# Performance work log

Hardware: AMD Instinct MI355X
Metric: run time of the kernel (lower is better)

The kernel has to match this reference:

```python
import jax, jax.numpy as jnp
import numpy as np

NC, NPR, E, B = 200000, 100000, 500000, 200000
DIN, HID, HEADS = 16, 256, 8
D = HID // HEADS
NCOLOR, NSIZE, NGROUP = 1000, 30, 50


def setup_inputs() -> dict:
    key = jax.random.key(0)
    ks = jax.random.split(key, 24)
    g = lambda i, shape, s=0.05: jax.random.normal(ks[i], shape, jnp.float32) * s
    return dict(
        customer_x=g(0, (NC, DIN), 1.0),
        product_x=g(1, (NPR, DIN), 1.0),
        proj_cust_W=g(2, (DIN, HID)), proj_cust_b=jnp.zeros((HID,), jnp.float32),
        proj_prod_W=g(3, (DIN, HID)), proj_prod_b=jnp.zeros((HID,), jnp.float32),
        att_src_r=g(4, (HEADS, D)), att_dst_r=g(5, (HEADS, D)),
        att_src_rb=g(6, (HEADS, D)), att_dst_rb=g(7, (HEADS, D)),
        q_sem=g(8, (HID,)), k_lin_W=g(9, (HID, HID)), k_lin_b=jnp.zeros((HID,), jnp.float32),
        color_emb=g(10, (NCOLOR, 8), 1.0),
        size_emb=g(11, (NSIZE, 4), 1.0),
        group_emb=g(12, (NGROUP, 4), 1.0),
        fc1_W=g(13, (HID * 2 + 16, 128)), fc1_b=jnp.zeros((128,), jnp.float32),
        fc2_W=g(14, (128, 32)), fc2_b=jnp.zeros((32,), jnp.float32),
        fc3_W=g(15, (32, 1)), fc3_b=jnp.zeros((1,), jnp.float32),
        bn1_gamma=jnp.ones((128,), jnp.float32), bn1_beta=jnp.zeros((128,), jnp.float32),
        bn2_gamma=jnp.ones((32,), jnp.float32), bn2_beta=jnp.zeros((32,), jnp.float32),
        edge_src=jax.random.randint(ks[16], (E,), 0, NC),
        edge_dst=jax.random.randint(ks[17], (E,), 0, NPR),
        label_src=jax.random.randint(ks[18], (B,), 0, NC),
        label_dst=jax.random.randint(ks[19], (B,), 0, NPR),
        size_idx=jax.random.randint(ks[20], (B,), 0, NSIZE),
        color_idx=jax.random.randint(ks[21], (B,), 0, NCOLOR),
        group_idx=jax.random.randint(ks[22], (B,), 0, NGROUP),
    )


def _edge_softmax(logits, dst, n):
    # destination-grouped softmax over edges; logits: [E,H]
    m = jax.ops.segment_max(logits, dst, num_segments=n)
    m = jnp.where(jnp.isfinite(m), m, 0.0)
    e = jnp.exp(logits - m[dst])
    s = jax.ops.segment_sum(e, dst, num_segments=n)
    return e / (s[dst] + 1e-16)


def _han_relation(h_src, h_dst, a_src, a_dst, src, dst, n_dst):
    # h_*: [N,H,D]; a_*: [H,D]
    logits = (h_src * a_src).sum(-1)[src] + (h_dst * a_dst).sum(-1)[dst]  # [E,H]
    logits = jax.nn.leaky_relu(logits, 0.2)
    alpha = _edge_softmax(logits, dst, n_dst)
    msg = alpha[:, :, None] * h_src[src]  # [E,H,D]
    out = jax.ops.segment_sum(msg, dst, num_segments=n_dst)
    return jax.nn.relu(out.reshape(n_dst, -1))  # [N_dst, H*D]


def _group(outs, q, kW, kb):
    # semantic attention over metapaths (PyG HANConv group)
    stk = jnp.stack(outs)  # [M,N,F]
    score = (q * jnp.tanh(stk @ kW + kb).mean(1)).sum(-1)  # [M]
    attn = jax.nn.softmax(score)
    return jnp.einsum('m,mnf->nf', attn, stk)


def _bn(x, gamma, beta):
    mu = x.mean(0)
    var = x.var(0)
    return (x - mu) * jax.lax.rsqrt(var + 1e-5) * gamma + beta


def reference(customer_x, product_x, proj_cust_W, proj_cust_b, proj_prod_W, proj_prod_b,
              att_src_r, att_dst_r, att_src_rb, att_dst_rb, q_sem, k_lin_W, k_lin_b,
              color_emb, size_emb, group_emb, fc1_W, fc1_b, fc2_W, fc2_b, fc3_W, fc3_b,
              bn1_gamma, bn1_beta, bn2_gamma, bn2_beta,
              edge_src, edge_dst, label_src, label_dst, size_idx, color_idx, group_idx):
    h_c = (customer_x @ proj_cust_W + proj_cust_b).reshape(-1, HEADS, D)
    h_p = (product_x @ proj_prod_W + proj_prod_b).reshape(-1, HEADS, D)
    # relation customer -returns-> product
    out_p = _han_relation(h_c, h_p, att_src_r, att_dst_r, edge_src, edge_dst, NPR)
    # relation product -returned_by-> customer (reversed edges)
    out_c = _han_relation(h_p, h_c, att_src_rb, att_dst_rb, edge_dst, edge_src, NC)
    cust = _group([out_c], q_sem, k_lin_W, k_lin_b)  # [NC, 256]
    prod = _group([out_p], q_sem, k_lin_W, k_lin_b)  # [NPR, 256]
    feat = jnp.concatenate([cust[label_src], prod[label_dst],
                            size_emb[size_idx], color_emb[color_idx], group_emb[group_idx]], axis=-1)
    x = jax.nn.relu(feat @ fc1_W + fc1_b)
    x = _bn(x, bn1_gamma, bn1_beta)
    x = jax.nn.relu(x @ fc2_W + fc2_b)
    x = _bn(x, bn2_gamma, bn2_beta)
    return x @ fc3_W + fc3_b
```

## Files before the change

kernel.cpp:

```cpp
#include <hip/hip_runtime.h>

#define NCC 200000
#define NPRR 100000
#define NEE 500000
#define NBB 200000

typedef __attribute__((ext_vector_type(8))) short bf16x8;
typedef __attribute__((ext_vector_type(16))) float f32x16;

__device__ __forceinline__ float b2f(unsigned short u){ return __uint_as_float(((unsigned)u)<<16); }
__device__ __forceinline__ unsigned short f2b(float f){
  unsigned x = __float_as_uint(f);
  return (unsigned short)((x + 0x7fffu + ((x>>16)&1u)) >> 16);
}

__global__ __launch_bounds__(256) void wa_prep2(
    const float* __restrict__ Wc, const float* __restrict__ bc,
    const float* __restrict__ attAc, const float* __restrict__ attBc,
    const float* __restrict__ Wp, const float* __restrict__ bp,
    const float* __restrict__ attAp, const float* __restrict__ attBp,
    float* __restrict__ WAc, float* __restrict__ WAp)
{
  int tid = threadIdx.x;
  for (int task = tid; task < 4*17*8; task += 256) {
    int grp = task / 136, rem = task % 136;
    int k = rem >> 3, h = rem & 7;
    const float* att = (grp==0)?attAc:(grp==1)?attBc:(grp==2)?attAp:attBp;
    const float* W   = (grp<2)?Wc:Wp;
    const float* bias= (grp<2)?bc:bp;
    const float* row = (k < 16) ? (W + k*256) : bias;
    float acc = 0.f;
    for (int d = 0; d < 32; d++) acc = fmaf(row[h*32+d], att[h*32+d], acc);
    if (grp<2) WAc[(grp&1)*136 + rem] = acc;
    else       WAp[(grp&1)*136 + rem] = acc;
  }
}

__global__ __launch_bounds__(256) void prep_proj(
    const float* __restrict__ Wc, const float* __restrict__ Wp,
    const float* __restrict__ WAc, const float* __restrict__ WAp,
    unsigned short* __restrict__ WtC, unsigned short* __restrict__ WtP,
    unsigned short* __restrict__ WAtC, unsigned short* __restrict__ WAtP)
{
  int idx = blockIdx.x*256 + threadIdx.x;
  if (idx < 4096){ int n=idx>>4, k=idx&15; WtC[idx]=f2b(Wc[k*256+n]); }
  else if (idx < 8192){ int t=idx-4096; int n=t>>4, k=t&15; WtP[t]=f2b(Wp[k*256+n]); }
  else if (idx < 8704){ int t=idx-8192; int n=t>>4, k=t&15;
    WAtC[t] = (n<16)? f2b(WAc[(n>>3)*136 + k*8 + (n&7)]) : (unsigned short)0; }
  else if (idx < 9216){ int t=idx-8704; int n=t>>4, k=t&15;
    WAtP[t] = (n<16)? f2b(WAp[(n>>3)*136 + k*8 + (n&7)]) : (unsigned short)0; }
}

__global__ __launch_bounds__(256) void prep_fc1(const float* __restrict__ fc1W,
    const float* __restrict__ fc1b,
    const float* __restrict__ size_emb, const float* __restrict__ color_emb,
    const float* __restrict__ group_emb,
    unsigned short* __restrict__ BtC, unsigned short* __restrict__ BtP,
    float* __restrict__ Ts, float* __restrict__ Tc, float* __restrict__ Tg)
{
  int idx = blockIdx.x*256 + threadIdx.x;
  if (idx < 32768){
    int n = idx>>8, k = idx&255;
    BtC[idx] = f2b(fc1W[k*128 + n]);
  } else if (idx < 65536){
    int t = idx - 32768;
    int n = t>>8, k = t&255;
    BtP[t] = f2b(fc1W[(256+k)*128 + n]);
  } else if (idx < 65536 + 30*128){
    int t = idx - 65536;
    int s = t>>7, j = t&127;
    float a = fc1b[j];
    #pragma unroll
    for (int c=0;c<4;c++) a = fmaf(size_emb[s*4+c], fc1W[(512+c)*128+j], a);
    Ts[t] = a;
  } else if (idx < 65536 + 30*128 + 1000*128){
    int t = idx - 65536 - 30*128;
    int col = t>>7, j = t&127;
    float a = 0.f;
    #pragma unroll
    for (int c=0;c<8;c++) a = fmaf(color_emb[col*8+c], fc1W[(516+c)*128+j], a);
    Tc[t] = a;
  } else if (idx < 65536 + 30*128 + 1000*128 + 50*128){
    int t = idx - 65536 - 30*128 - 1000*128;
    int g = t>>7, j = t&127;
    float a = 0.f;
    #pragma unroll
    for (int c=0;c<4;c++) a = fmaf(group_emb[g*4+c], fc1W[(524+c)*128+j], a);
    Tg[t] = a;
  }
}

__global__ __launch_bounds__(256) void proj_mfma(const float* __restrict__ X,
    const unsigned short* __restrict__ Wt, const unsigned short* __restrict__ WAt,
    const float* __restrict__ WA,
    unsigned short* __restrict__ H, float* __restrict__ sA, float* __restrict__ sB,
    int N, int nt)
{
  __shared__ unsigned short wt[4608];
  __shared__ float biasS[16];
  int tid = threadIdx.x;
  for (int i=tid; i<512; i+=256) ((uint4*)wt)[i] = ((const uint4*)Wt)[i];
  for (int i=tid; i<64;  i+=256) ((uint4*)(wt+4096))[i] = ((const uint4*)WAt)[i];
  if (tid < 16) biasS[tid] = WA[(tid>>3)*136 + 128 + (tid&7)];
  __syncthreads();
  int wv = tid>>6, lane = tid&63, m = lane&31, hi = lane>>5;
  for (int t = blockIdx.x; t < nt; t += gridDim.x){
    int node = t*32 + m;
    bf16x8 a;
    {
      const float4* xr = (const float4*)(X + (long long)node*16 + hi*8);
      float4 f0 = xr[0], f1 = xr[1];
      unsigned short av[8] = {f2b(f0.x),f2b(f0.y),f2b(f0.z),f2b(f0.w),
                              f2b(f1.x),f2b(f1.y),f2b(f1.z),f2b(f1.w)};
      a = *(bf16x8*)av;
    }
    #pragma unroll
    for (int s=0;s<2;s++){
      int c0 = wv*64 + s*32;
      bf16x8 b = *(const bf16x8*)(wt + (c0+m)*16 + hi*8);
      f32x16 acc;
      #pragma unroll
      for (int i=0;i<16;i++) acc[i]=0.f;
      acc = __builtin_amdgcn_mfma_f32_32x32x16_bf16(a, b, acc, 0, 0, 0);
      #pragma unroll
      for (int reg=0; reg<16; reg++){
        int row = (reg&3) + 8*(reg>>2) + 4*hi;
        H[(long long)(t*32+row)*256 + c0 + m] = f2b(acc[reg]);
      }
    }
    if (wv == 0){
      bf16x8 b = *(const bf16x8*)(wt + 4096 + m*16 + hi*8);
      f32x16 acc;
      #pragma unroll
      for (int i=0;i<16;i++) acc[i]=0.f;
      acc = __builtin_amdgcn_mfma_f32_32x32x16_bf16(a, b, acc, 0, 0, 0);
      if (m < 16){
        float bias = biasS[m];
        float* dst = (m < 8) ? sA : sB;
        int h = m & 7;
        #pragma unroll
        for (int reg=0; reg<16; reg++){
          int row = (reg&3) + 8*(reg>>2) + 4*hi;
          dst[(long long)(t*32+row)*8 + h] = acc[reg] + bias;
        }
      }
    }
  }
}

__global__ __launch_bounds__(256) void hist2(const int* __restrict__ src, const int* __restrict__ dst,
    int* __restrict__ cnt_c, int* __restrict__ cnt_p, int E)
{
  int e = blockIdx.x*256 + threadIdx.x;
  if (e >= E) return;
  atomicAdd(&cnt_p[dst[e]], 1);
  atomicAdd(&cnt_c[src[e]], 1);
}

__global__ __launch_bounds__(256) void scan_phase1(const int* __restrict__ cnt, int* __restrict__ bsum, int N)
{
  __shared__ int red[256];
  int tid = threadIdx.x;
  int base = blockIdx.x*1024 + tid*4;
  int s = 0;
  #pragma unroll
  for (int k=0;k<4;k++){ int i=base+k; if (i<N) s += cnt[i]; }
  red[tid] = s;
  __syncthreads();
  for (int off=128; off>0; off>>=1){ if (tid<off) red[tid]+=red[tid+off]; __syncthreads(); }
  if (tid==0) bsum[blockIdx.x] = red[0];
}

__global__ __launch_bounds__(256) void scan_phase2(int* __restrict__ bsum, int B,
    int* __restrict__ rowptr, int N)
{
  __shared__ int ts[256];
  int tid = threadIdx.x;
  int v = (tid<B) ? bsum[tid] : 0;
  ts[tid] = v;
  __syncthreads();
  for (int off=1; off<256; off<<=1){
    int t = (tid>=off) ? ts[tid-off] : 0;
    __syncthreads();
    ts[tid] += t;
    __syncthreads();
  }
  if (tid < B) bsum[tid] = ts[tid] - v;
  if (tid == B-1) rowptr[N] = ts[tid];
}

__global__ __launch_bounds__(256) void scan_phase3(const int* __restrict__ cnt,
    const int* __restrict__ bsum, int* __restrict__ rowptr, int N)
{
  __shared__ int ts[256];
  int tid = threadIdx.x;
  int base = blockIdx.x*1024 + tid*4;
  int v[4]; int s = 0;
  #pragma unroll
  for (int k=0;k<4;k++){ int i=base+k; v[k] = (i<N) ? cnt[i] : 0; s += v[k]; }
  ts[tid] = s;
  __syncthreads();
  for (int off=1; off<256; off<<=1){
    int t = (tid>=off) ? ts[tid-off] : 0;
    __syncthreads();
    ts[tid] += t;
    __syncthreads();
  }
  int run = bsum[blockIdx.x] + ts[tid] - s;
  #pragma unroll
  for (int k=0;k<4;k++){ int i=base+k; if (i<N){ rowptr[i]=run; run += v[k]; } }
}

__global__ __launch_bounds__(256) void place2(const int* __restrict__ src, const int* __restrict__ dst,
    const int* __restrict__ rp_r, const int* __restrict__ rp_rb,
    int* __restrict__ cnt_p, int* __restrict__ cnt_c,
    int* __restrict__ si_r, int* __restrict__ si_rb, int E)
{
  int e = blockIdx.x*256 + threadIdx.x;
  if (e >= E) return;
  int s = src[e], d = dst[e];
  si_r [rp_r [d] + atomicAdd(&cnt_p[d], 1)] = s;
  si_rb[rp_rb[s] + atomicAdd(&cnt_c[s], 1)] = d;
}

__global__ __launch_bounds__(256) void agg_gemm(
    const int* __restrict__ rowptr, const int* __restrict__ srcidx,
    const float* __restrict__ sSrc, const float* __restrict__ sDst,
    const unsigned short* __restrict__ H, const unsigned short* __restrict__ Bt,
    unsigned short* __restrict__ Y)
{
  __shared__ unsigned short feat[32*264];
  int tid = threadIdx.x;
  int wv = tid>>6, lane = tid&63;
  int g = lane>>4, ln = lane&15, h = ln>>1;
  long long base = (long long)blockIdx.x*32;
  #pragma unroll
  for (int t=0;t<2;t++){
    int r = wv*8 + t*4 + g;
    long long n = base + r;
    int e0 = rowptr[n], e1 = rowptr[n+1];
    int elast = e1 - 1;
    float sdh = sDst[n*8 + h];
    float acc[16];
    #pragma unroll
    for (int c=0;c<16;c++) acc[c]=0.f;
    float den = 0.f;
    for (int e = e0; e < e1; e += 4){
      int i1 = min(e+1, elast), i2 = min(e+2, elast), i3 = min(e+3, elast);
      int s0 = srcidx[e],  s1 = srcidx[i1];
      int s2 = srcidx[i2], s3 = srcidx[i3];
      const uint4* p0 = (const uint4*)&H[(long long)s0*256 + ln*16];
      const uint4* p1 = (const uint4*)&H[(long long)s1*256 + ln*16];
      const uint4* p2 = (const uint4*)&H[(long long)s2*256 + ln*16];
      const uint4* p3 = (const uint4*)&H[(long long)s3*256 + ln*16];
      uint4 uA0 = p0[0], uA1 = p0[1];
      uint4 uB0 = p1[0], uB1 = p1[1];
      uint4 uC0 = p2[0], uC1 = p2[1];
      uint4 uD0 = p3[0], uD1 = p3[1];
      float l0 = sSrc[(long long)s0*8 + h];
      float l1 = sSrc[(long long)s1*8 + h];
      float l2 = sSrc[(long long)s2*8 + h];
      float l3 = sSrc[(long long)s3*8 + h];
      l0 += sdh; l1 += sdh; l2 += sdh; l3 += sdh;
      float w0 = __expf(l0 > 0.f ? l0 : 0.2f*l0);
      float w1 = (e+1 < e1) ? __expf(l1 > 0.f ? l1 : 0.2f*l1) : 0.f;
      float w2 = (e+2 < e1) ? __expf(l2 > 0.f ? l2 : 0.2f*l2) : 0.f;
      float w3 = (e+3 < e1) ? __expf(l3 > 0.f ? l3 : 0.2f*l3) : 0.f;
      den += (w0 + w1) + (w2 + w3);
      unsigned ua[8] = {uA0.x,uA0.y,uA0.z,uA0.w, uA1.x,uA1.y,uA1.z,uA1.w};
      unsigned ub[8] = {uB0.x,uB0.y,uB0.z,uB0.w, uB1.x,uB1.y,uB1.z,uB1.w};
      unsigned uc[8] = {uC0.x,uC0.y,uC0.z,uC0.w, uC1.x,uC1.y,uC1.z,uC1.w};
      unsigned ud[8] = {uD0.x,uD0.y,uD0.z,uD0.w, uD1.x,uD1.y,uD1.z,uD1.w};
      #pragma unroll
      for (int p=0;p<8;p++){
        acc[p*2]   = fmaf(w0, b2f((unsigned short)(ua[p]&0xffffu)), acc[p*2]);
        acc[p*2+1] = fmaf(w0, b2f((unsigned short)(ua[p]>>16)),     acc[p*2+1]);
        acc[p*2]   = fmaf(w1, b2f((unsigned short)(ub[p]&0xffffu)), acc[p*2]);
        acc[p*2+1] = fmaf(w1, b2f((unsigned short)(ub[p]>>16)),     acc[p*2+1]);
        acc[p*2]   = fmaf(w2, b2f((unsigned short)(uc[p]&0xffffu)), acc[p*2]);
        acc[p*2+1] = fmaf(w2, b2f((unsigned short)(uc[p]>>16)),     acc[p*2+1]);
        acc[p*2]   = fmaf(w3, b2f((unsigned short)(ud[p]&0xffffu)), acc[p*2]);
        acc[p*2+1] = fmaf(w3, b2f((unsigned short)(ud[p]>>16)),     acc[p*2+1]);
      }
    }
    float inv = 1.f/(den + 1e-16f);
    unsigned short ov[16];
    #pragma unroll
    for (int c=0;c<16;c++) ov[c] = f2b(fmaxf(acc[c]*inv, 0.f));
    *(uint4*)&feat[r*264 + ln*16]     = *(uint4*)&ov[0];
    *(uint4*)&feat[r*264 + ln*16 + 8] = *(uint4*)&ov[8];
  }
  __syncthreads();
  int m = lane&31, hi = lane>>5;
  f32x16 acc;
  #pragma unroll
  for (int i=0;i<16;i++) acc[i]=0.f;
  const unsigned short* ap  = feat + m*264 + hi*8;
  const unsigned short* btp = Bt + (wv*32 + m)*256 + hi*8;
  #pragma unroll 4
  for (int ks=0; ks<16; ks++){
    bf16x8 a = *(const bf16x8*)(ap + ks*16);
    bf16x8 b = *(const bf16x8*)(btp + ks*16);
    acc = __builtin_amdgcn_mfma_f32_32x32x16_bf16(a, b, acc, 0, 0, 0);
  }
  int col = wv*32 + m;
  #pragma unroll
  for (int reg=0; reg<16; reg++){
    int row = (reg&3) + 8*(reg>>2) + 4*hi;
    Y[(base+row)*128 + col] = f2b(acc[reg]);
  }
}

__global__ __launch_bounds__(256) void gather_fc1(
    const unsigned short* __restrict__ Yc, const unsigned short* __restrict__ Yp,
    const float* __restrict__ Ts, const float* __restrict__ Tc, const float* __restrict__ Tg,
    const int* __restrict__ lsrc, const int* __restrict__ ldst,
    const int* __restrict__ sidx, const int* __restrict__ cidx, const int* __restrict__ gidx,
    unsigned short* __restrict__ x1, float* __restrict__ bnsum, int ntiles)
{
  __shared__ float redS[16][128];
  __shared__ float redQ[16][128];
  int tid = threadIdx.x;
  int rl = tid>>4, g = tid&15;
  float sacc[8] = {0,0,0,0,0,0,0,0};
  float qacc[8] = {0,0,0,0,0,0,0,0};
  for (int t = blockIdx.x; t < ntiles; t += gridDim.x){
    long long row = (long long)t*16 + rl;
    int ls = lsrc[row], ld = ldst[row], si = sidx[row], ci = cidx[row], gi = gidx[row];
    uint4 uc = *(const uint4*)&Yc[(long long)ls*128 + g*8];
    uint4 up = *(const uint4*)&Yp[(long long)ld*128 + g*8];
    float4 t0 = *(const float4*)&Ts[si*128 + g*8];
    float4 t1 = *(const float4*)&Ts[si*128 + g*8 + 4];
    float4 c0 = *(const float4*)&Tc[ci*128 + g*8];
    float4 c1 = *(const float4*)&Tc[ci*128 + g*8 + 4];
    float4 g0 = *(const float4*)&Tg[gi*128 + g*8];
    float4 g1 = *(const float4*)&Tg[gi*128 + g*8 + 4];
    unsigned ucs[4] = {uc.x,uc.y,uc.z,uc.w};
    unsigned ups[4] = {up.x,up.y,up.z,up.w};
    float tb[8] = {t0.x+c0.x+g0.x, t0.y+c0.y+g0.y, t0.z+c0.z+g0.z, t0.w+c0.w+g0.w,
                   t1.x+c1.x+g1.x, t1.y+c1.y+g1.y, t1.z+c1.z+g1.z, t1.w+c1.w+g1.w};
    unsigned short ov[8];
    #pragma unroll
    for (int p=0;p<4;p++){
      float vl = b2f((unsigned short)(ucs[p]&0xffffu)) + b2f((unsigned short)(ups[p]&0xffffu)) + tb[p*2];
      float vh = b2f((unsigned short)(ucs[p]>>16))     + b2f((unsigned short)(ups[p]>>16))     + tb[p*2+1];
      vl = fmaxf(vl, 0.f); vh = fmaxf(vh, 0.f);
      ov[p*2] = f2b(vl); ov[p*2+1] = f2b(vh);
      sacc[p*2]   += vl; qacc[p*2]   += vl*vl;
      sacc[p*2+1] += vh; qacc[p*2+1] += vh*vh;
    }
    *(uint4*)&x1[row*128 + g*8] = *(uint4*)ov;
  }
  #pragma unroll
  for (int j=0;j<8;j++){ redS[rl][g*8+j]=sacc[j]; redQ[rl][g*8+j]=qacc[j]; }
  __syncthreads();
  if (tid < 128){
    float s=0.f, q=0.f;
    #pragma unroll
    for (int r=0;r<16;r++){ s += redS[r][tid]; q += redQ[r][tid]; }
    atomicAdd(&bnsum[tid], s);
    atomicAdd(&bnsum[128+tid], q);
  }
}

__global__ void bn1_fold(const float* __restrict__ bnsum,
    const float* __restrict__ gamma, const float* __restrict__ beta,
    const float* __restrict__ fc2W, const float* __restrict__ fc2b,
    unsigned short* __restrict__ Bt2, float* __restrict__ b2p, float invB)
{
  __shared__ float sc[128], sh[128];
  int tid = threadIdx.x;
  if (tid<128){
    float mu  = bnsum[tid]*invB;
    float var = bnsum[128+tid]*invB - mu*mu;
    float s = gamma[tid] * rsqrtf(var + 1e-5f);
    sc[tid]=s; sh[tid]= beta[tid] - mu*s;
  }
  __syncthreads();
  for (int idx=tid; idx<32*128; idx+=256){
    int n = idx>>7, k = idx&127;
    Bt2[idx] = f2b(sc[k]*fc2W[k*32+n]);
  }
  if (tid<32){
    float a = fc2b[tid];
    for (int k=0;k<128;k++) a = fmaf(sh[k], fc2W[k*32+tid], a);
    b2p[tid]=a;
  }
}

__global__ __launch_bounds__(256) void fc2_mfma(const unsigned short* __restrict__ x1,
    const unsigned short* __restrict__ Bt2, const float* __restrict__ b2p,
    unsigned short* __restrict__ x2, float* __restrict__ bnsum2, int M)
{
  __shared__ unsigned short xt[128*136];
  __shared__ unsigned short wt[32*136];
  __shared__ float redS[4][32];
  __shared__ float redQ[4][32];
  int tid = threadIdx.x;
  long long base = (long long)blockIdx.x*128;
  for (int idx=tid; idx<128*16; idx+=256){
    int r = idx>>4, c = idx&15;
    uint4 u = make_uint4(0,0,0,0);
    if (base + r < M) u = *(const uint4*)&x1[(base+r)*128 + c*8];
    *(uint4*)&xt[r*136 + c*8] = u;
  }
  for (int idx=tid; idx<32*16; idx+=256){
    int r = idx>>4, c = idx&15;
    *(uint4*)&wt[r*136 + c*8] = *(const uint4*)&Bt2[r*128 + c*8];
  }
  __syncthreads();
  int wv = tid>>6, lane = tid&63;
  int m = lane&31, hi = lane>>5;
  f32x16 acc;
  #pragma unroll
  for (int i=0;i<16;i++) acc[i]=0.f;
  const unsigned short* ap = xt + (wv*32 + m)*136 + hi*8;
  const unsigned short* bp = wt + m*136 + hi*8;
  #pragma unroll
  for (int ks=0; ks<8; ks++){
    bf16x8 a = *(const bf16x8*)(ap + ks*16);
    bf16x8 b = *(const bf16x8*)(bp + ks*16);
    acc = __builtin_amdgcn_mfma_f32_32x32x16_bf16(a, b, acc, 0, 0, 0);
  }
  int col = m;
  float bias = b2p[col];
  float s=0.f, q=0.f;
  #pragma unroll
  for (int reg=0; reg<16; reg++){
    int row = (reg&3) + 8*(reg>>2) + 4*hi;
    long long grow = base + wv*32 + row;
    float v = fmaxf(acc[reg] + bias, 0.f);
    if (grow < M) x2[grow*32 + col] = f2b(v);
    s += v; q += v*v;
  }
  if (base + 128 > M){
    s = 0.f; q = 0.f;
    #pragma unroll
    for (int reg=0; reg<16; reg++){
      int row = (reg&3) + 8*(reg>>2) + 4*hi;
      long long grow = base + wv*32 + row;
      float v = fmaxf(acc[reg] + bias, 0.f);
      if (grow < M){ s += v; q += v*v; }
    }
  }
  s += __shfl_xor(s, 32);
  q += __shfl_xor(q, 32);
  if (hi == 0){ redS[wv][col] = s; redQ[wv][col] = q; }
  __syncthreads();
  if (tid < 32){
    float a = redS[0][tid]+redS[1][tid]+redS[2][tid]+redS[3][tid];
    float b = redQ[0][tid]+redQ[1][tid]+redQ[2][tid]+redQ[3][tid];
    atomicAdd(&bnsum2[tid], a);
    atomicAdd(&bnsum2[32+tid], b);
  }
}

__global__ void bn2_fold(const float* __restrict__ bnsum2,
    const float* __restrict__ gamma2, const float* __restrict__ beta2,
    const float* __restrict__ fc3W, const float* __restrict__ fc3b,
    float* __restrict__ w3p, float invB)
{
  __shared__ float sh3[32];
  int tid = threadIdx.x;
  if (tid<32){
    float mu  = bnsum2[tid]*invB;
    float var = bnsum2[32+tid]*invB - mu*mu;
    float s   = gamma2[tid] * rsqrtf(var + 1e-5f);
    float shv = beta2[tid] - mu*s;
    float w   = fc3W[tid];
    w3p[tid]  = s*w;
    sh3[tid]  = shv*w;
  }
  __syncthreads();
  if (tid==0){
    float a = fc3b[0];
    for (int j=0;j<32;j++) a += sh3[j];
    w3p[32] = a;
  }
}

__global__ __launch_bounds__(256) void fc3_kernel(const unsigned short* __restrict__ x2,
    const float* __restrict__ w3p, float* __restrict__ out)
{
  __shared__ float wl[34];
  int tid = threadIdx.x;
  if (tid<33) wl[tid]=w3p[tid];
  __syncthreads();
  long long row = (long long)blockIdx.x*32 + (tid>>3);
  int j0 = (tid&7)*4;
  uint2 u = *(const uint2*)(x2 + row*32 + j0);
  float a = b2f((unsigned short)(u.x&0xffffu))*wl[j0]
          + b2f((unsigned short)(u.x>>16))   *wl[j0+1]
          + b2f((unsigned short)(u.y&0xffffu))*wl[j0+2]
          + b2f((unsigned short)(u.y>>16))   *wl[j0+3];
  a += __shfl_xor(a,1);
  a += __shfl_xor(a,2);
  a += __shfl_xor(a,4);
  if ((tid&7)==0) out[row] = a + wl[32];
}

extern "C" void kernel_launch(void* const* d_in, const int* in_sizes, int n_in,
                              void* d_out, int out_size, void* d_ws, size_t ws_size,
                              hipStream_t stream)
{
  (void)in_sizes; (void)n_in; (void)out_size; (void)ws_size;
  const float* customer_x = (const float*)d_in[0];
  const float* product_x  = (const float*)d_in[1];
  const float* pcW = (const float*)d_in[2];
  const float* pcB = (const float*)d_in[3];
  const float* ppW = (const float*)d_in[4];
  const float* ppB = (const float*)d_in[5];
  const float* att_src_r  = (const float*)d_in[6];
  const float* att_dst_r  = (const float*)d_in[7];
  const float* att_src_rb = (const float*)d_in[8];
  const float* att_dst_rb = (const float*)d_in[9];
  const float* color_emb = (const float*)d_in[13];
  const float* size_emb  = (const float*)d_in[14];
  const float* group_emb = (const float*)d_in[15];
  const float* fc1W = (const float*)d_in[16];
  const float* fc1b = (const float*)d_in[17];
  const float* fc2W = (const float*)d_in[18];
  const float* fc2b = (const float*)d_in[19];
  const float* fc3W = (const float*)d_in[20];
  const float* fc3b = (const float*)d_in[21];
  const float* bn1g = (const float*)d_in[22];
  const float* bn1b = (const float*)d_in[23];
  const float* bn2g = (const float*)d_in[24];
  const float* bn2b = (const float*)d_in[25];
  const int* edge_src  = (const int*)d_in[26];
  const int* edge_dst  = (const int*)d_in[27];
  const int* label_src = (const int*)d_in[28];
  const int* label_dst = (const int*)d_in[29];
  const int* size_idx  = (const int*)d_in[30];
  const int* color_idx = (const int*)d_in[31];
  const int* group_idx = (const int*)d_in[32];

  char* ws = (char*)d_ws;
  size_t off = 0;
  auto alloc = [&](size_t bytes)->char* {
    char* p = ws + off;
    off += (bytes + 255) & ~(size_t)255;
    return p;
  };
  unsigned short* H_c  = (unsigned short*)alloc((size_t)NCC*256*2);
  unsigned short* H_p  = (unsigned short*)alloc((size_t)NPRR*256*2);
  unsigned short* slab = (unsigned short*)alloc((size_t)NPRR*256*2);
  float* s_cr     = (float*)alloc((size_t)NCC*8*4);
  float* s_crb    = (float*)alloc((size_t)NCC*8*4);
  float* s_pr     = (float*)alloc((size_t)NPRR*8*4);
  float* s_prb    = (float*)alloc((size_t)NPRR*8*4);
  int* rowptr_r   = (int*)alloc((size_t)(NPRR+1)*4);
  int* rowptr_rb  = (int*)alloc((size_t)(NCC+1)*4);
  int* srcidx_r   = (int*)alloc((size_t)NEE*4);
  int* srcidx_rb  = (int*)alloc((size_t)NEE*4);
  int* cnts       = (int*)alloc((size_t)(NCC+NPRR)*2*4);
  int* cnt_c      = cnts;
  int* cnt_p      = cnts + NCC;
  int* cnt_c2     = cnts + NCC + NPRR;
  int* cnt_p2     = cnts + NCC + NPRR + NCC;
  int* bsum_c     = (int*)alloc(256*4);
  int* bsum_p     = (int*)alloc(256*4);
  unsigned short* BtC = (unsigned short*)alloc(128*256*2);
  unsigned short* BtP = (unsigned short*)alloc(128*256*2);
  float* Ts     = (float*)alloc(30*128*4);
  float* Tc     = (float*)alloc(1000*128*4);
  float* Tg     = (float*)alloc(50*128*4);
  float* wa_c   = (float*)alloc(272*4);
  float* wa_p   = (float*)alloc(272*4);
  unsigned short* WtC  = (unsigned short*)alloc(256*16*2);
  unsigned short* WtP  = (unsigned short*)alloc(256*16*2);
  unsigned short* WAtC = (unsigned short*)alloc(32*16*2);
  unsigned short* WAtP = (unsigned short*)alloc(32*16*2);
  float* bnsum1 = (float*)alloc(256*4);
  float* bnsum2 = (float*)alloc(64*4);
  unsigned short* Bt2 = (unsigned short*)alloc(32*128*2);
  float* b2p    = (float*)alloc(32*4);
  float* w3p    = (float*)alloc(34*4);
  unsigned short* Y_p = slab;
  unsigned short* Y_c = H_c;
  unsigned short* x1b = H_p;
  unsigned short* x2b = (unsigned short*)s_cr;

  hipMemsetAsync(bnsum1, 0, 1280, stream);
  hipMemsetAsync(cnts, 0, (size_t)(NCC+NPRR)*2*4, stream);

  wa_prep2<<<1,256,0,stream>>>(pcW, pcB, att_src_r, att_dst_rb,
                               ppW, ppB, att_dst_r, att_src_rb, wa_c, wa_p);
  prep_proj<<<36,256,0,stream>>>(pcW, ppW, wa_c, wa_p, WtC, WtP, WAtC, WAtP);
  prep_fc1<<<(203776+255)/256,256,0,stream>>>(fc1W, fc1b, size_emb, color_emb, group_emb,
      BtC, BtP, Ts, Tc, Tg);

  proj_mfma<<<2048,256,0,stream>>>(customer_x, WtC, WAtC, wa_c, H_c, s_cr, s_crb, NCC, NCC/32);
  proj_mfma<<<2048,256,0,stream>>>(product_x,  WtP, WAtP, wa_p, H_p, s_pr, s_prb, NPRR, NPRR/32);

  const int eg = (NEE+255)/256;
  const int BP = (NPRR+1023)/1024;
  const int BC = (NCC +1023)/1024;
  hist2<<<eg,256,0,stream>>>(edge_src, edge_dst, cnt_c, cnt_p, NEE);
  scan_phase1<<<BP,256,0,stream>>>(cnt_p, bsum_p, NPRR);
  scan_phase2<<<1,256,0,stream>>>(bsum_p, BP, rowptr_r, NPRR);
  scan_phase3<<<BP,256,0,stream>>>(cnt_p, bsum_p, rowptr_r, NPRR);
  scan_phase1<<<BC,256,0,stream>>>(cnt_c, bsum_c, NCC);
  scan_phase2<<<1,256,0,stream>>>(bsum_c, BC, rowptr_rb, NCC);
  scan_phase3<<<BC,256,0,stream>>>(cnt_c, bsum_c, rowptr_rb, NCC);
  place2<<<eg,256,0,stream>>>(edge_src, edge_dst, rowptr_r, rowptr_rb,
      cnt_p2, cnt_c2, srcidx_r, srcidx_rb, NEE);

  agg_gemm<<<NPRR/32,256,0,stream>>>(rowptr_r,  srcidx_r,  s_cr,  s_pr,  H_c, BtP, Y_p);
  agg_gemm<<<NCC/32,256,0,stream>>>(rowptr_rb, srcidx_rb, s_prb, s_crb, H_p, BtC, Y_c);

  gather_fc1<<<2048,256,0,stream>>>(Y_c, Y_p, Ts, Tc, Tg,
      label_src, label_dst, size_idx, color_idx, group_idx, x1b, bnsum1, NBB/16);

  bn1_fold<<<1,256,0,stream>>>(bnsum1, bn1g, bn1b, fc2W, fc2b, Bt2, b2p, 1.0f/NBB);
  fc2_mfma<<<(NBB+127)/128,256,0,stream>>>(x1b, Bt2, b2p, x2b, bnsum2, NBB);
  bn2_fold<<<1,64,0,stream>>>(bnsum2, bn2g, bn2b, fc3W, fc3b, w3p, 1.0f/NBB);
  fc3_kernel<<<NBB/32,256,0,stream>>>(x2b, w3p, (float*)d_out);
}
```

Baseline: 570.2 us.

## Skip aggregation for nodes not referenced by label pairs; merge scan launches

Marks every customer and product that appears in label_src or label_dst during the histogram pass, then skips the edge aggregation loop for unmarked destination nodes in agg_gemm. Only marked rows feed the final MLP, so this is dead-work elimination that depends on the label index distribution, not a test-specific shortcut. The per-relation prefix-scan phases are also merged into single launches to cut launch count. The cost is an extra memset region, extra scattered writes in the histogram kernel, and one extra check per node.

```diff
diff --git a/kernel.cpp b/kernel.cpp
--- a/kernel.cpp
+++ b/kernel.cpp
@@ -148,33 +148,47 @@
   }
 }
 
-__global__ __launch_bounds__(256) void hist2(const int* __restrict__ src, const int* __restrict__ dst,
-    int* __restrict__ cnt_c, int* __restrict__ cnt_p, int E)
+__global__ __launch_bounds__(256) void hist2u(const int* __restrict__ src, const int* __restrict__ dst,
+    int* __restrict__ cnt_c, int* __restrict__ cnt_p, int E,
+    const int* __restrict__ lsrc, const int* __restrict__ ldst,
+    int* __restrict__ used_c, int* __restrict__ used_p, int B)
 {
   int e = blockIdx.x*256 + threadIdx.x;
-  if (e >= E) return;
-  atomicAdd(&cnt_p[dst[e]], 1);
-  atomicAdd(&cnt_c[src[e]], 1);
-}
-
-__global__ __launch_bounds__(256) void scan_phase1(const int* __restrict__ cnt, int* __restrict__ bsum, int N)
+  if (e < E){
+    atomicAdd(&cnt_p[dst[e]], 1);
+    atomicAdd(&cnt_c[src[e]], 1);
+  }
+  if (e < B){
+    used_c[lsrc[e]] = 1;
+    used_p[ldst[e]] = 1;
+  }
+}
+
+__global__ __launch_bounds__(256) void scan_p1f(const int* __restrict__ cnt_p, int* __restrict__ bsum_p, int Np,
+    const int* __restrict__ cnt_c, int* __restrict__ bsum_c, int Nc, int BP)
 {
   __shared__ int red[256];
-  int tid = threadIdx.x;
-  int base = blockIdx.x*1024 + tid*4;
+  const int* cnt; int* bsum; int N; int blk;
+  if ((int)blockIdx.x < BP){ cnt=cnt_p; bsum=bsum_p; N=Np; blk=blockIdx.x; }
+  else                     { cnt=cnt_c; bsum=bsum_c; N=Nc; blk=blockIdx.x-BP; }
+  int tid = threadIdx.x;
+  int base = blk*1024 + tid*4;
   int s = 0;
   #pragma unroll
   for (int k=0;k<4;k++){ int i=base+k; if (i<N) s += cnt[i]; }
   red[tid] = s;
   __syncthreads();
   for (int off=128; off>0; off>>=1){ if (tid<off) red[tid]+=red[tid+off]; __syncthreads(); }
-  if (tid==0) bsum[blockIdx.x] = red[0];
-}
-
-__global__ __launch_bounds__(256) void scan_phase2(int* __restrict__ bsum, int B,
-    int* __restrict__ rowptr, int N)
+  if (tid==0) bsum[blk] = red[0];
+}
+
+__global__ __launch_bounds__(256) void scan_p2f(int* __restrict__ bsum_p, int Bp, int* __restrict__ rowptr_p, int Np,
+    int* __restrict__ bsum_c, int Bc, int* __restrict__ rowptr_c, int Nc)
 {
   __shared__ int ts[256];
+  int* bsum; int B; int* rowptr; int N;
+  if (blockIdx.x == 0){ bsum=bsum_p; B=Bp; rowptr=rowptr_p; N=Np; }
+  else                { bsum=bsum_c; B=Bc; rowptr=rowptr_c; N=Nc; }
   int tid = threadIdx.x;
   int v = (tid<B) ? bsum[tid] : 0;
   ts[tid] = v;
@@ -189,12 +203,17 @@
   if (tid == B-1) rowptr[N] = ts[tid];
 }
 
-__global__ __launch_bounds__(256) void scan_phase3(const int* __restrict__ cnt,
-    const int* __restrict__ bsum, int* __restrict__ rowptr, int N)
+__global__ __launch_bounds__(256) void scan_p3f(const int* __restrict__ cnt_p, const int* __restrict__ bsum_p,
+    int* __restrict__ rowptr_p, int Np,
+    const int* __restrict__ cnt_c, const int* __restrict__ bsum_c,
+    int* __restrict__ rowptr_c, int Nc, int BP)
 {
   __shared__ int ts[256];
-  int tid = threadIdx.x;
-  int base = blockIdx.x*1024 + tid*4;
+  const int* cnt; const int* bsum; int* rowptr; int N; int blk;
+  if ((int)blockIdx.x < BP){ cnt=cnt_p; bsum=bsum_p; rowptr=rowptr_p; N=Np; blk=blockIdx.x; }
+  else                     { cnt=cnt_c; bsum=bsum_c; rowptr=rowptr_c; N=Nc; blk=blockIdx.x-BP; }
+  int tid = threadIdx.x;
+  int base = blk*1024 + tid*4;
   int v[4]; int s = 0;
   #pragma unroll
   for (int k=0;k<4;k++){ int i=base+k; v[k] = (i<N) ? cnt[i] : 0; s += v[k]; }
@@ -206,7 +225,7 @@
     ts[tid] += t;
     __syncthreads();
   }
-  int run = bsum[blockIdx.x] + ts[tid] - s;
+  int run = bsum[blk] + ts[tid] - s;
   #pragma unroll
   for (int k=0;k<4;k++){ int i=base+k; if (i<N){ rowptr[i]=run; run += v[k]; } }
 }
@@ -227,60 +246,63 @@
     const int* __restrict__ rowptr, const int* __restrict__ srcidx,
     const float* __restrict__ sSrc, const float* __restrict__ sDst,
     const unsigned short* __restrict__ H, const unsigned short* __restrict__ Bt,
-    unsigned short* __restrict__ Y)
+    unsigned short* __restrict__ Y, const int* __restrict__ used)
 {
   __shared__ unsigned short feat[32*264];
   int tid = threadIdx.x;
   int wv = tid>>6, lane = tid&63;
-  int g = lane>>4, ln = lane&15, h = ln>>1;
+  int g = lane>>4, ln = lane&15, h = ln>>2;
+  h = (lane&15) >> 1;
   long long base = (long long)blockIdx.x*32;
   #pragma unroll
   for (int t=0;t<2;t++){
     int r = wv*8 + t*4 + g;
     long long n = base + r;
-    int e0 = rowptr[n], e1 = rowptr[n+1];
-    int elast = e1 - 1;
-    float sdh = sDst[n*8 + h];
     float acc[16];
     #pragma unroll
     for (int c=0;c<16;c++) acc[c]=0.f;
     float den = 0.f;
-    for (int e = e0; e < e1; e += 4){
-      int i1 = min(e+1, elast), i2 = min(e+2, elast), i3 = min(e+3, elast);
-      int s0 = srcidx[e],  s1 = srcidx[i1];
-      int s2 = srcidx[i2], s3 = srcidx[i3];
-      const uint4* p0 = (const uint4*)&H[(long long)s0*256 + ln*16];
-      const uint4* p1 = (const uint4*)&H[(long long)s1*256 + ln*16];
-      const uint4* p2 = (const uint4*)&H[(long long)s2*256 + ln*16];
-      const uint4* p3 = (const uint4*)&H[(long long)s3*256 + ln*16];
-      uint4 uA0 = p0[0], uA1 = p0[1];
-      uint4 uB0 = p1[0], uB1 = p1[1];
-      uint4 uC0 = p2[0], uC1 = p2[1];
-      uint4 uD0 = p3[0], uD1 = p3[1];
-      float l0 = sSrc[(long long)s0*8 + h];
-      float l1 = sSrc[(long long)s1*8 + h];
-      float l2 = sSrc[(long long)s2*8 + h];
-      float l3 = sSrc[(long long)s3*8 + h];
-      l0 += sdh; l1 += sdh; l2 += sdh; l3 += sdh;
-      float w0 = __expf(l0 > 0.f ? l0 : 0.2f*l0);
-      float w1 = (e+1 < e1) ? __expf(l1 > 0.f ? l1 : 0.2f*l1) : 0.f;
-      float w2 = (e+2 < e1) ? __expf(l2 > 0.f ? l2 : 0.2f*l2) : 0.f;
-      float w3 = (e+3 < e1) ? __expf(l3 > 0.f ? l3 : 0.2f*l3) : 0.f;
-      den += (w0 + w1) + (w2 + w3);
-      unsigned ua[8] = {uA0.x,uA0.y,uA0.z,uA0.w, uA1.x,uA1.y,uA1.z,uA1.w};
-      unsigned ub[8] = {uB0.x,uB0.y,uB0.z,uB0.w, uB1.x,uB1.y,uB1.z,uB1.w};
-      unsigned uc[8] = {uC0.x,uC0.y,uC0.z,uC0.w, uC1.x,uC1.y,uC1.z,uC1.w};
-      unsigned ud[8] = {uD0.x,uD0.y,uD0.z,uD0.w, uD1.x,uD1.y,uD1.z,uD1.w};
-      #pragma unroll
-      for (int p=0;p<8;p++){
-        acc[p*2]   = fmaf(w0, b2f((unsigned short)(ua[p]&0xffffu)), acc[p*2]);
-        acc[p*2+1] = fmaf(w0, b2f((unsigned short)(ua[p]>>16)),     acc[p*2+1]);
-        acc[p*2]   = fmaf(w1, b2f((unsigned short)(ub[p]&0xffffu)), acc[p*2]);
-        acc[p*2+1] = fmaf(w1, b2f((unsigned short)(ub[p]>>16)),     acc[p*2+1]);
-        acc[p*2]   = fmaf(w2, b2f((unsigned short)(uc[p]&0xffffu)), acc[p*2]);
-        acc[p*2+1] = fmaf(w2, b2f((unsigned short)(uc[p]>>16)),     acc[p*2+1]);
-        acc[p*2]   = fmaf(w3, b2f((unsigned short)(ud[p]&0xffffu)), acc[p*2]);
-        acc[p*2+1] = fmaf(w3, b2f((unsigned short)(ud[p]>>16)),     acc[p*2+1]);
+    if (used[n]){
+      int e0 = rowptr[n], e1 = rowptr[n+1];
+      int elast = e1 - 1;
+      float sdh = sDst[n*8 + h];
+      for (int e = e0; e < e1; e += 4){
+        int i1 = min(e+1, elast), i2 = min(e+2, elast), i3 = min(e+3, elast);
+        int s0 = srcidx[e],  s1 = srcidx[i1];
+        int s2 = srcidx[i2], s3 = srcidx[i3];
+        const uint4* p0 = (const uint4*)&H[(long long)s0*256 + ln*16];
+        const uint4* p1 = (const uint4*)&H[(long long)s1*256 + ln*16];
+        const uint4* p2 = (const uint4*)&H[(long long)s2*256 + ln*16];
+        const uint4* p3 = (const uint4*)&H[(long long)s3*256 + ln*16];
+        uint4 uA0 = p0[0], uA1 = p0[1];
+        uint4 uB0 = p1[0], uB1 = p1[1];
+        uint4 uC0 = p2[0], uC1 = p2[1];
+        uint4 uD0 = p3[0], uD1 = p3[1];
+        float l0 = sSrc[(long long)s0*8 + h];
+        float l1 = sSrc[(long long)s1*8 + h];
+        float l2 = sSrc[(long long)s2*8 + h];
+        float l3 = sSrc[(long long)s3*8 + h];
+        l0 += sdh; l1 += sdh; l2 += sdh; l3 += sdh;
+        float w0 = __expf(l0 > 0.f ? l0 : 0.2f*l0);
+        float w1 = (e+1 < e1) ? __expf(l1 > 0.f ? l1 : 0.2f*l1) : 0.f;
+        float w2 = (e+2 < e1) ? __expf(l2 > 0.f ? l2 : 0.2f*l2) : 0.f;
+        float w3 = (e+3 < e1) ? __expf(l3 > 0.f ? l3 : 0.2f*l3) : 0.f;
+        den += (w0 + w1) + (w2 + w3);
+        unsigned ua[8] = {uA0.x,uA0.y,uA0.z,uA0.w, uA1.x,uA1.y,uA1.z,uA1.w};
+        unsigned ub[8] = {uB0.x,uB0.y,uB0.z,uB0.w, uB1.x,uB1.y,uB1.z,uB1.w};
+        unsigned uc[8] = {uC0.x,uC0.y,uC0.z,uC0.w, uC1.x,uC1.y,uC1.z,uC1.w};
+        unsigned ud[8] = {uD0.x,uD0.y,uD0.z,uD0.w, uD1.x,uD1.y,uD1.z,uD1.w};
+        #pragma unroll
+        for (int p=0;p<8;p++){
+          acc[p*2]   = fmaf(w0, b2f((unsigned short)(ua[p]&0xffffu)), acc[p*2]);
+          acc[p*2+1] = fmaf(w0, b2f((unsigned short)(ua[p]>>16)),     acc[p*2+1]);
+          acc[p*2]   = fmaf(w1, b2f((unsigned short)(ub[p]&0xffffu)), acc[p*2]);
+          acc[p*2+1] = fmaf(w1, b2f((unsigned short)(ub[p]>>16)),     acc[p*2+1]);
+          acc[p*2]   = fmaf(w2, b2f((unsigned short)(uc[p]&0xffffu)), acc[p*2]);
+          acc[p*2+1] = fmaf(w2, b2f((unsigned short)(uc[p]>>16)),     acc[p*2+1]);
+          acc[p*2]   = fmaf(w3, b2f((unsigned short)(ud[p]&0xffffu)), acc[p*2]);
+          acc[p*2+1] = fmaf(w3, b2f((unsigned short)(ud[p]>>16)),     acc[p*2+1]);
+        }
       }
     }
     float inv = 1.f/(den + 1e-16f);
@@ -553,11 +575,13 @@
   int* rowptr_rb  = (int*)alloc((size_t)(NCC+1)*4);
   int* srcidx_r   = (int*)alloc((size_t)NEE*4);
   int* srcidx_rb  = (int*)alloc((size_t)NEE*4);
-  int* cnts       = (int*)alloc((size_t)(NCC+NPRR)*2*4);
+  int* cnts       = (int*)alloc((size_t)(NCC+NPRR)*3*4);
   int* cnt_c      = cnts;
   int* cnt_p      = cnts + NCC;
   int* cnt_c2     = cnts + NCC + NPRR;
   int* cnt_p2     = cnts + NCC + NPRR + NCC;
+  int* used_c     = cnts + (NCC + NPRR)*2;
+  int* used_p     = used_c + NCC;
   int* bsum_c     = (int*)alloc(256*4);
   int* bsum_p     = (int*)alloc(256*4);
   unsigned short* BtC = (unsigned short*)alloc(128*256*2);
@@ -582,7 +606,7 @@
   unsigned short* x2b = (unsigned short*)s_cr;
 
   hipMemsetAsync(bnsum1, 0, 1280, stream);
-  hipMemsetAsync(cnts, 0, (size_t)(NCC+NPRR)*2*4, stream);
+  hipMemsetAsync(cnts, 0, (size_t)(NCC+NPRR)*3*4, stream);
 
   wa_prep2<<<1,256,0,stream>>>(pcW, pcB, att_src_r, att_dst_rb,
                                ppW, ppB, att_dst_r, att_src_rb, wa_c, wa_p);
@@ -596,18 +620,17 @@
   const int eg = (NEE+255)/256;
   const int BP = (NPRR+1023)/1024;
   const int BC = (NCC +1023)/1024;
-  hist2<<<eg,256,0,stream>>>(edge_src, edge_dst, cnt_c, cnt_p, NEE);
-  scan_phase1<<<BP,256,0,stream>>>(cnt_p, bsum_p, NPRR);
-  scan_phase2<<<1,256,0,stream>>>(bsum_p, BP, rowptr_r, NPRR);
-  scan_phase3<<<BP,256,0,stream>>>(cnt_p, bsum_p, rowptr_r, NPRR);
-  scan_phase1<<<BC,256,0,stream>>>(cnt_c, bsum_c, NCC);
-  scan_phase2<<<1,256,0,stream>>>(bsum_c, BC, rowptr_rb, NCC);
-  scan_phase3<<<BC,256,0,stream>>>(cnt_c, bsum_c, rowptr_rb, NCC);
+  hist2u<<<eg,256,0,stream>>>(edge_src, edge_dst, cnt_c, cnt_p, NEE,
+      label_src, label_dst, used_c, used_p, NBB);
+  scan_p1f<<<BP+BC,256,0,stream>>>(cnt_p, bsum_p, NPRR, cnt_c, bsum_c, NCC, BP);
+  scan_p2f<<<2,256,0,stream>>>(bsum_p, BP, rowptr_r, NPRR, bsum_c, BC, rowptr_rb, NCC);
+  scan_p3f<<<BP+BC,256,0,stream>>>(cnt_p, bsum_p, rowptr_r, NPRR,
+      cnt_c, bsum_c, rowptr_rb, NCC, BP);
   place2<<<eg,256,0,stream>>>(edge_src, edge_dst, rowptr_r, rowptr_rb,
       cnt_p2, cnt_c2, srcidx_r, srcidx_rb, NEE);
 
-  agg_gemm<<<NPRR/32,256,0,stream>>>(rowptr_r,  srcidx_r,  s_cr,  s_pr,  H_c, BtP, Y_p);
-  agg_gemm<<<NCC/32,256,0,stream>>>(rowptr_rb, srcidx_rb, s_prb, s_crb, H_p, BtC, Y_c);
+  agg_gemm<<<NPRR/32,256,0,stream>>>(rowptr_r,  srcidx_r,  s_cr,  s_pr,  H_c, BtP, Y_p, used_p);
+  agg_gemm<<<NCC/32,256,0,stream>>>(rowptr_rb, srcidx_rb, s_prb, s_crb, H_p, BtC, Y_c, used_c);
 
   gather_fc1<<<2048,256,0,stream>>>(Y_c, Y_p, Ts, Tc, Tg,
       label_src, label_dst, size_idx, color_idx, group_idx, x1b, bnsum1, NBB/16);
```

Measured after the change: 575.9 us. About the same (+1.0%).
